# Kernel optimization log

Hardware: AMD Instinct MI355X
Metric: run time of the kernel (lower is better)

The kernel has to match this reference:

```python
import jax, jax.numpy as jnp
import numpy as np

B, S, H, HD = 2, 2048, 16, 128
HID = H * HD            # 2048
FF = 4 * HID            # 8192
ROT = int(HD * 0.25)    # 32 rotary dims (rotary_pct=0.25)
EPS = 1e-5
ROPE_BASE = 10000.0


def _layernorm(x, g, b):
    mu = jnp.mean(x, axis=-1, keepdims=True)
    var = jnp.mean(jnp.square(x - mu), axis=-1, keepdims=True)
    return (x - mu) * jax.lax.rsqrt(var + EPS) * g + b


def _rope_cos_sin(seq_len, dim, dtype):
    inv_freq = 1.0 / (ROPE_BASE ** (np.arange(0, dim, 2, dtype=np.float32) / dim))
    t = np.arange(seq_len, dtype=np.float32)
    freqs = np.outer(t, inv_freq)              # [S, dim/2]
    emb = np.concatenate([freqs, freqs], -1)   # [S, dim]
    return jnp.asarray(np.cos(emb), dtype), jnp.asarray(np.sin(emb), dtype)


def _apply_rope(x, cos, sin):
    # x: [B, H, S, ROT]; GPTNeoX rotate_half
    half = x.shape[-1] // 2
    x1, x2 = x[..., :half], x[..., half:]
    rot = jnp.concatenate([-x2, x1], axis=-1)
    return x * cos[None, None, :, :] + rot * sin[None, None, :, :]


def setup_inputs() -> dict:
    key = jax.random.key(0)
    ks = jax.random.split(key, 8)
    f = jnp.float32
    return {
        "hidden_states": jax.random.normal(ks[0], (B, S, HID), f),
        "ln1_g": jnp.ones((HID,), f), "ln1_b": jnp.zeros((HID,), f),
        "ln2_g": jnp.ones((HID,), f), "ln2_b": jnp.zeros((HID,), f),
        "W_qkv": jax.random.normal(ks[1], (HID, 3 * HID), f) * 0.02,
        "b_qkv": jnp.zeros((3 * HID,), f),
        "W_o": jax.random.normal(ks[2], (HID, HID), f) * 0.02,
        "b_o": jnp.zeros((HID,), f),
        "W_fc": jax.random.normal(ks[3], (HID, FF), f) * 0.02,
        "b_fc": jnp.zeros((FF,), f),
        "W_proj": jax.random.normal(ks[4], (FF, HID), f) * 0.02,
        "b_proj": jnp.zeros((HID,), f),
    }


def reference(hidden_states, ln1_g, ln1_b, ln2_g, ln2_b,
              W_qkv, b_qkv, W_o, b_o, W_fc, b_fc, W_proj, b_proj):
    dtype = hidden_states.dtype
    x = _layernorm(hidden_states, ln1_g, ln1_b)

    # fused QKV, GPTNeoX per-head interleaved layout [B,S,H,3*HD]
    qkv = (x @ W_qkv + b_qkv).reshape(B, S, H, 3 * HD)
    q = jnp.transpose(qkv[..., :HD], (0, 2, 1, 3))          # [B,H,S,HD]
    k = jnp.transpose(qkv[..., HD:2 * HD], (0, 2, 1, 3))
    v = jnp.transpose(qkv[..., 2 * HD:], (0, 2, 1, 3))

    cos, sin = _rope_cos_sin(S, ROT, dtype)
    q = jnp.concatenate([_apply_rope(q[..., :ROT], cos, sin), q[..., ROT:]], -1)
    k = jnp.concatenate([_apply_rope(k[..., :ROT], cos, sin), k[..., ROT:]], -1)

    # eager attention: scores / sqrt(hd), causal mask-fill, softmax, matmul
    scale = 1.0 / jnp.sqrt(jnp.asarray(HD, dtype))
    scores = jnp.einsum("bhqd,bhkd->bhqk", q, k) * scale
    causal = jnp.tril(jnp.ones((S, S), bool))
    scores = jnp.where(causal, scores, jnp.finfo(dtype).min)
    weights = jax.nn.softmax(scores, axis=-1)
    ctx = jnp.einsum("bhqk,bhkd->bhqd", weights, v)          # [B,H,S,HD]
    ctx = jnp.transpose(ctx, (0, 2, 1, 3)).reshape(B, S, HID)
    attn_out = ctx @ W_o + b_o

    # parallel residual: mlp(ln2(h)) + attn(ln1(h)) + h
    m = _layernorm(hidden_states, ln2_g, ln2_b)
    mlp_out = jax.nn.gelu(m @ W_fc + b_fc, approximate=False) @ W_proj + b_proj
    return mlp_out + attn_out + hidden_states
```

## Files before the change

### kernel.cpp

```cpp
#include <hip/hip_runtime.h>
#include <hip/hip_bf16.h>
#include <math.h>

#define BDIM 2
#define SDIM 2048
#define HDIM 16
#define HD 128
#define HID 2048
#define FFD 8192
#define NTOK (BDIM*SDIM)
#define QKVW (3*HID)

typedef __hip_bfloat16 bf16;
typedef __attribute__((ext_vector_type(8))) short short8;
typedef __attribute__((ext_vector_type(4))) short short4_;
typedef __attribute__((ext_vector_type(4))) float floatx4;

__device__ inline short bfbits(float f) {
  bf16 h = __float2bfloat16(f);
  short s;
  __builtin_memcpy(&s, &h, 2);
  return s;
}

__global__ __launch_bounds__(256) void transpose_cvt(
    const float* __restrict__ W, bf16* __restrict__ Wt, int K, int N)
{
  __shared__ float tile[32][33];
  int n0 = blockIdx.x * 32, k0 = blockIdx.y * 32;
  int tx = threadIdx.x, ty = threadIdx.y;
  #pragma unroll
  for (int r = ty; r < 32; r += 8)
    tile[r][tx] = W[(size_t)(k0 + r) * N + n0 + tx];
  __syncthreads();
  #pragma unroll
  for (int r = ty; r < 32; r += 8)
    Wt[(size_t)(n0 + r) * K + k0 + tx] = __float2bfloat16(tile[tx][r]);
}

__global__ __launch_bounds__(256) void ln_both(
    const float* __restrict__ x,
    const float* __restrict__ g1, const float* __restrict__ b1,
    const float* __restrict__ g2, const float* __restrict__ b2,
    bf16* __restrict__ o1, bf16* __restrict__ o2)
{
  int row = blockIdx.x;
  int tid = threadIdx.x;
  const float4* xr = (const float4*)(x + (size_t)row * HID);
  float4 va = xr[tid], vb = xr[tid + 256];
  float s = va.x + va.y + va.z + va.w + vb.x + vb.y + vb.z + vb.w;
  float q = va.x*va.x + va.y*va.y + va.z*va.z + va.w*va.w
          + vb.x*vb.x + vb.y*vb.y + vb.z*vb.z + vb.w*vb.w;
  #pragma unroll
  for (int off = 1; off < 64; off <<= 1) {
    s += __shfl_xor(s, off);
    q += __shfl_xor(q, off);
  }
  __shared__ float red[8];
  int wave = tid >> 6;
  if ((tid & 63) == 0) { red[wave] = s; red[4 + wave] = q; }
  __syncthreads();
  s = red[0] + red[1] + red[2] + red[3];
  q = red[4] + red[5] + red[6] + red[7];
  float mu = s * (1.0f / HID);
  float var = q * (1.0f / HID) - mu * mu;
  float rs = rsqrtf(var + 1e-5f);

  const float4* g1v = (const float4*)g1; const float4* b1v = (const float4*)b1;
  const float4* g2v = (const float4*)g2; const float4* b2v = (const float4*)b2;
  short4_* o1v = (short4_*)(o1 + (size_t)row * HID);
  short4_* o2v = (short4_*)(o2 + (size_t)row * HID);
  #pragma unroll
  for (int p = 0; p < 2; ++p) {
    int e = tid + p * 256;
    float4 xv = (p == 0) ? va : vb;
    float4 gv = g1v[e], bv = b1v[e];
    short4_ pk;
    pk[0] = bfbits((xv.x - mu) * rs * gv.x + bv.x);
    pk[1] = bfbits((xv.y - mu) * rs * gv.y + bv.y);
    pk[2] = bfbits((xv.z - mu) * rs * gv.z + bv.z);
    pk[3] = bfbits((xv.w - mu) * rs * gv.w + bv.w);
    o1v[e] = pk;
    gv = g2v[e]; bv = b2v[e];
    pk[0] = bfbits((xv.x - mu) * rs * gv.x + bv.x);
    pk[1] = bfbits((xv.y - mu) * rs * gv.y + bv.y);
    pk[2] = bfbits((xv.z - mu) * rs * gv.z + bv.z);
    pk[3] = bfbits((xv.w - mu) * rs * gv.w + bv.w);
    o2v[e] = pk;
  }
}

template<int EPI>
__global__ __launch_bounds__(512, 2) void gemm8(
    const bf16* __restrict__ A, const bf16* __restrict__ Bt,
    const float* __restrict__ bias,
    float* __restrict__ Cf, bf16* __restrict__ Cb,
    const bf16* __restrict__ r1b, const float* __restrict__ r2,
    int M, int N, int K)
{
  __shared__ bf16 SA[4][256 * 32];
  __shared__ bf16 SB[4][256 * 32];
  const int tid = threadIdx.x;
  const int wave = tid >> 6, lane = tid & 63;
  const int quad = lane >> 4, l16 = lane & 15;
  const int wr = wave >> 2, wc = wave & 3;

  const int nwg = gridDim.x * gridDim.y;
  const int flat = blockIdx.y * gridDim.x + blockIdx.x;
  const int swz = (flat & 7) * (nwg >> 3) + (flat >> 3);
  const int bx = swz % gridDim.x, by = swz / gridDim.x;
  const int n0 = bx * 256, m0 = by * 256;

  const int stg_r = wave * 16 + (lane >> 2);
  const int stg_c8 = (((lane & 3) ^ ((lane >> 3) & 3)) << 3);
  const bf16* stgA = A + (size_t)(m0 + stg_r) * K + stg_c8;
  const bf16* stgB = Bt + (size_t)(n0 + stg_r) * K + stg_c8;
  const int ldsOff = wave * 16 * 32;

  const int rd_sw = ((quad ^ ((l16 >> 1) & 3)) << 3);
  const int rdA = (wr * 128 + l16) * 32 + rd_sw;
  const int rdB = (wc * 64 + l16) * 32 + rd_sw;

  floatx4 acc[8][4];
  #pragma unroll
  for (int i = 0; i < 8; ++i)
    #pragma unroll
    for (int j = 0; j < 4; ++j) acc[i][j] = (floatx4)0.0f;

  const int KT = K >> 5;

#define STAGE_A8(KT3) { const int b_ = (KT3) & 3;                              \
  __builtin_amdgcn_global_load_lds(                                            \
      (const __attribute__((address_space(1))) void*)(stgA + (size_t)(KT3)*32),\
      (__attribute__((address_space(3))) void*)&SA[b_][ldsOff], 16, 0, 0);     \
  __builtin_amdgcn_global_load_lds(                                            \
      (const __attribute__((address_space(1))) void*)(stgA + (size_t)128*K + (size_t)(KT3)*32), \
      (__attribute__((address_space(3))) void*)&SA[b_][128*32 + ldsOff], 16, 0, 0); }
#define STAGE_B8(KT3) { const int b_ = (KT3) & 3;                              \
  __builtin_amdgcn_global_load_lds(                                            \
      (const __attribute__((address_space(1))) void*)(stgB + (size_t)(KT3)*32),\
      (__attribute__((address_space(3))) void*)&SB[b_][ldsOff], 16, 0, 0);     \
  __builtin_amdgcn_global_load_lds(                                            \
      (const __attribute__((address_space(1))) void*)(stgB + (size_t)128*K + (size_t)(KT3)*32), \
      (__attribute__((address_space(3))) void*)&SB[b_][128*32 + ldsOff], 16, 0, 0); }

  STAGE_A8(0); STAGE_B8(0);
  STAGE_A8(1); STAGE_B8(1);
  STAGE_A8(2); STAGE_B8(2);
  asm volatile("s_waitcnt vmcnt(8)" ::: "memory");
  __builtin_amdgcn_s_barrier();

  short8 av[4], bv[4];
  for (int kt = 0; kt < KT; ++kt) {
    const bf16* as_ = &SA[kt & 3][0];
    const bf16* bs_ = &SB[kt & 3][0];
    const bool st = (kt + 3) < KT;

    #pragma unroll
    for (int i = 0; i < 4; ++i) av[i] = *(const short8*)&as_[rdA + i * 512];
    #pragma unroll
    for (int j = 0; j < 4; ++j) bv[j] = *(const short8*)&bs_[rdB + j * 512];
    if (st) STAGE_A8(kt + 3);
    __builtin_amdgcn_s_barrier();
    asm volatile("s_waitcnt lgkmcnt(0)" ::: "memory");
    __builtin_amdgcn_sched_barrier(0);
    __builtin_amdgcn_s_setprio(1);
    #pragma unroll
    for (int i = 0; i < 4; ++i)
      #pragma unroll
      for (int j = 0; j < 4; ++j)
        acc[i][j] = __builtin_amdgcn_mfma_f32_16x16x32_bf16(av[i], bv[j], acc[i][j], 0, 0, 0);
    __builtin_amdgcn_s_setprio(0);
    __builtin_amdgcn_s_barrier();

    #pragma unroll
    for (int i = 0; i < 4; ++i) av[i] = *(const short8*)&as_[rdA + 2048 + i * 512];
    if (st) STAGE_B8(kt + 3);
    __builtin_amdgcn_s_barrier();
    asm volatile("s_waitcnt lgkmcnt(0)" ::: "memory");
    __builtin_amdgcn_sched_barrier(0);
    __builtin_amdgcn_s_setprio(1);
    #pragma unroll
    for (int i = 0; i < 4; ++i)
      #pragma unroll
      for (int j = 0; j < 4; ++j)
        acc[4 + i][j] = __builtin_amdgcn_mfma_f32_16x16x32_bf16(av[i], bv[j], acc[4 + i][j], 0, 0, 0);
    __builtin_amdgcn_s_setprio(0);

    if (st) {
      asm volatile("s_waitcnt vmcnt(8)" ::: "memory");
    } else if (kt + 3 == KT) {
      asm volatile("s_waitcnt vmcnt(4)" ::: "memory");
    } else if (kt + 2 == KT) {
      asm volatile("s_waitcnt vmcnt(0)" ::: "memory");
    }
    if (kt + 1 < KT) __builtin_amdgcn_s_barrier();
  }
#undef STAGE_A8
#undef STAGE_B8

  #pragma unroll
  for (int i = 0; i < 8; ++i) {
    #pragma unroll
    for (int j = 0; j < 4; ++j) {
      int col = n0 + wc * 64 + j * 16 + l16;
      float bsv = bias[col];
      #pragma unroll
      for (int r = 0; r < 4; ++r) {
        int row = m0 + wr * 128 + i * 16 + quad * 4 + r;
        size_t idx = (size_t)row * N + col;
        float v = acc[i][j][r] + bsv;
        if (EPI == 1) {
          v = 0.5f * v * (1.0f + erff(v * 0.70710678118654752f));
          Cb[idx] = __float2bfloat16(v);
        } else if (EPI == 2) {
          Cf[idx] = v + __bfloat162float(r1b[idx]) + r2[idx];
        } else {
          Cb[idx] = __float2bfloat16(v);
        }
      }
    }
  }
}

__global__ __launch_bounds__(256) void rope_vt(
    bf16* __restrict__ qkv, bf16* __restrict__ vT)
{
  int bh = blockIdx.x, s0 = blockIdx.y * 32;
  int b = bh >> 4, h = bh & 15;
  int tid = threadIdx.x;
  __shared__ bf16 vs[32][136];
  const float qsc = 0.12751740f;

  for (int idx = tid; idx < 512; idx += 256) {
    int sl = idx >> 4, d = idx & 15;
    int s = s0 + sl;
    bf16* base = qkv + (size_t)(b * SDIM + s) * QKVW + h * 384;
    float fr = (float)s * expf(-(float)d * 0.5756462732485114f);
    float c = cosf(fr), sn = sinf(fr);
    float q1 = __bfloat162float(base[d]);
    float q2 = __bfloat162float(base[d + 16]);
    float k1 = __bfloat162float(base[128 + d]);
    float k2 = __bfloat162float(base[128 + d + 16]);
    base[d]        = __float2bfloat16(qsc * (q1 * c - q2 * sn));
    base[d + 16]   = __float2bfloat16(qsc * (q2 * c + q1 * sn));
    base[128 + d]      = __float2bfloat16(k1 * c - k2 * sn);
    base[128 + d + 16] = __float2bfloat16(k2 * c + k1 * sn);
  }
  for (int idx = tid; idx < 32 * 96; idx += 256) {
    int sl = idx / 96, d = 32 + idx % 96;
    bf16* base = qkv + (size_t)(b * SDIM + s0 + sl) * QKVW + h * 384;
    base[d] = __float2bfloat16(qsc * __bfloat162float(base[d]));
  }

  for (int idx = tid; idx < 32 * 128; idx += 256) {
    int sl = idx >> 7, d = idx & 127;
    vs[sl][d] = qkv[(size_t)(b * SDIM + s0 + sl) * QKVW + h * 384 + 256 + d];
  }
  __syncthreads();
  for (int idx = tid; idx < 32 * 128; idx += 256) {
    int d = idx >> 5, sl = idx & 31;
    vT[((size_t)bh * HD + d) * SDIM + s0 + sl] = vs[sl][d];
  }
}

#define LOAD_K(KB, K0) { \
  int krow_ = (K0); \
  _Pragma("unroll") for (int nh_ = 0; nh_ < 2; ++nh_) \
    _Pragma("unroll") for (int c_ = 0; c_ < 4; ++c_) \
      KB[nh_*4+c_] = *(const short8*)&Kb[(size_t)(krow_ + nh_*16 + l16) * QKVW + c_*32 + quad*8]; }

#define SOFTMAX(S0, S1, MR, LR, OO, ROWQ, DOMASK, K0, SLOT) { \
  if (DOMASK) { \
    _Pragma("unroll") for (int r_ = 0; r_ < 4; ++r_) { \
      int row_ = (ROWQ) + quad*4 + r_; \
      S0[r_] = ((K0) + l16 <= row_) ? S0[r_] : -1e30f; \
      S1[r_] = ((K0) + 16 + l16 <= row_) ? S1[r_] : -1e30f; } } \
  _Pragma("unroll") for (int r_ = 0; r_ < 4; ++r_) { \
    float mx_ = fmaxf(S0[r_], S1[r_]); \
    mx_ = fmaxf(mx_, __shfl_xor(mx_, 1)); \
    mx_ = fmaxf(mx_, __shfl_xor(mx_, 2)); \
    mx_ = fmaxf(mx_, __shfl_xor(mx_, 4)); \
    mx_ = fmaxf(mx_, __shfl_xor(mx_, 8)); \
    float mnew_ = fmaxf(MR[r_], mx_); \
    float alpha_ = __builtin_amdgcn_exp2f(MR[r_] - mnew_); \
    MR[r_] = mnew_; \
    S0[r_] = __builtin_amdgcn_exp2f(S0[r_] - mnew_); \
    S1[r_] = __builtin_amdgcn_exp2f(S1[r_] - mnew_); \
    float sm_ = S0[r_] + S1[r_]; \
    sm_ += __shfl_xor(sm_, 1); sm_ += __shfl_xor(sm_, 2); \
    sm_ += __shfl_xor(sm_, 4); sm_ += __shfl_xor(sm_, 8); \
    LR[r_] = LR[r_] * alpha_ + sm_; \
    _Pragma("unroll") for (int d_ = 0; d_ < 8; ++d_) OO[d_][r_] *= alpha_; \
    Ps[wave][SLOT][quad*4 + r_][l16]      = __float2bfloat16(S0[r_]); \
    Ps[wave][SLOT][quad*4 + r_][16 + l16] = __float2bfloat16(S1[r_]); } }

#define FLASH_ITER(IT, KC, KN) { \
  const int k0_ = (IT) * 32; \
  const int k0n_ = ((IT) + 1 < nk) ? k0_ + 32 : 0; \
  LOAD_K(KN, k0n_); \
  short8 vbuf_[8]; \
  _Pragma("unroll") for (int d_ = 0; d_ < 8; ++d_) \
    vbuf_[d_] = *(const short8*)&Vb[(size_t)(d_*16 + l16) * SDIM + k0_ + quad*8]; \
  floatx4 scB_[2]; scB_[0] = (floatx4)0.0f; scB_[1] = (floatx4)0.0f; \
  _Pragma("unroll") for (int c_ = 0; c_ < 4; ++c_) { \
    scB_[0] = __builtin_amdgcn_mfma_f32_16x16x32_bf16(aqB[c_], KC[c_],   scB_[0], 0,0,0); \
    scB_[1] = __builtin_amdgcn_mfma_f32_16x16x32_bf16(aqB[c_], KC[4+c_], scB_[1], 0,0,0); } \
  const bool actA_ = (k0_ <= qa + 15); \
  floatx4 scA_[2]; scA_[0] = (floatx4)0.0f; scA_[1] = (floatx4)0.0f; \
  if (actA_) { \
    _Pragma("unroll") for (int c_ = 0; c_ < 4; ++c_) { \
      scA_[0] = __builtin_amdgcn_mfma_f32_16x16x32_bf16(aqA[c_], KC[c_],   scA_[0], 0,0,0); \
      scA_[1] = __builtin_amdgcn_mfma_f32_16x16x32_bf16(aqA[c_], KC[4+c_], scA_[1], 0,0,0); } } \
  SOFTMAX(scB_[0], scB_[1], mB, lB, oB, qb, (k0_ + 32 >= kmax), k0_, 0); \
  if (actA_) { \
    SOFTMAX(scA_[0], scA_[1], mA, lA, oA, qa, (k0_ + 32 > qa + 15), k0_, 1); \
    short8 pfB_ = *(const short8*)&Ps[wave][0][l16][quad*8]; \
    short8 pfA_ = *(const short8*)&Ps[wave][1][l16][quad*8]; \
    _Pragma("unroll") for (int d_ = 0; d_ < 8; ++d_) { \
      oB[d_] = __builtin_amdgcn_mfma_f32_16x16x32_bf16(pfB_, vbuf_[d_], oB[d_], 0,0,0); \
      oA[d_] = __builtin_amdgcn_mfma_f32_16x16x32_bf16(pfA_, vbuf_[d_], oA[d_], 0,0,0); } \
  } else { \
    short8 pfB_ = *(const short8*)&Ps[wave][0][l16][quad*8]; \
    _Pragma("unroll") for (int d_ = 0; d_ < 8; ++d_) \
      oB[d_] = __builtin_amdgcn_mfma_f32_16x16x32_bf16(pfB_, vbuf_[d_], oB[d_], 0,0,0); } }

__global__ __launch_bounds__(256) void flash_attn(
    const bf16* __restrict__ qkv, const bf16* __restrict__ vT,
    bf16* __restrict__ ctx)
{
  int bh = blockIdx.x;
  int b = bh >> 4, h = bh & 15;
  int tid = threadIdx.x;
  int wave = tid >> 6, lane = tid & 63;
  int quad = lane >> 4, l16 = lane & 15;
  int p = blockIdx.y * 4 + wave;
  int qa = 16 * p;
  int qb = SDIM - 16 * (p + 1);
  int kmax = qb + 16;
  int nk = (kmax + 31) >> 5;
  const bf16* Qb = qkv + (size_t)b * SDIM * QKVW + h * 384;
  const bf16* Kb = Qb + 128;
  const bf16* Vb = vT + (size_t)bh * HD * SDIM;
  __shared__ bf16 Ps[4][2][16][32];

  short8 aqA[4], aqB[4];
  #pragma unroll
  for (int c = 0; c < 4; ++c) {
    aqA[c] = *(const short8*)&Qb[(size_t)(qa + l16) * QKVW + c * 32 + quad * 8];
    aqB[c] = *(const short8*)&Qb[(size_t)(qb + l16) * QKVW + c * 32 + quad * 8];
  }

  floatx4 oA[8], oB[8];
  #pragma unroll
  for (int d = 0; d < 8; ++d) { oA[d] = (floatx4)0.0f; oB[d] = (floatx4)0.0f; }
  float mA[4] = {-INFINITY, -INFINITY, -INFINITY, -INFINITY};
  float mB[4] = {-INFINITY, -INFINITY, -INFINITY, -INFINITY};
  float lA[4] = {0.0f, 0.0f, 0.0f, 0.0f};
  float lB[4] = {0.0f, 0.0f, 0.0f, 0.0f};

  short8 kb0[8], kb1[8];
  LOAD_K(kb0, 0);
  for (int it = 0; it < nk; it += 2) {
    FLASH_ITER(it, kb0, kb1);
    if (it + 1 < nk) { FLASH_ITER(it + 1, kb1, kb0); }
  }

  float rlA[4], rlB[4];
  #pragma unroll
  for (int r = 0; r < 4; ++r) { rlA[r] = 1.0f / lA[r]; rlB[r] = 1.0f / lB[r]; }
  #pragma unroll
  for (int d = 0; d < 8; ++d) {
    #pragma unroll
    for (int r = 0; r < 4; ++r) {
      int rowA = qa + quad * 4 + r;
      int rowB = qb + quad * 4 + r;
      ctx[((size_t)b * SDIM + rowA) * HID + h * HD + d * 16 + l16] =
          __float2bfloat16(oA[d][r] * rlA[r]);
      ctx[((size_t)b * SDIM + rowB) * HID + h * HD + d * 16 + l16] =
          __float2bfloat16(oB[d][r] * rlB[r]);
    }
  }
}

extern "C" void kernel_launch(void* const* d_in, const int* in_sizes, int n_in,
                              void* d_out, int out_size, void* d_ws, size_t ws_size,
                              hipStream_t stream) {
  const float* hidden = (const float*)d_in[0];
  const float* ln1g = (const float*)d_in[1];
  const float* ln1b = (const float*)d_in[2];
  const float* ln2g = (const float*)d_in[3];
  const float* ln2b = (const float*)d_in[4];
  const float* Wqkv = (const float*)d_in[5];
  const float* bqkv = (const float*)d_in[6];
  const float* Wo   = (const float*)d_in[7];
  const float* bo   = (const float*)d_in[8];
  const float* Wfc  = (const float*)d_in[9];
  const float* bfc  = (const float*)d_in[10];
  const float* Wproj= (const float*)d_in[11];
  const float* bproj= (const float*)d_in[12];

  char* ws = (char*)d_ws;
  const size_t SZ_WQKV = (size_t)QKVW * HID * 2;
  const size_t SZ_WO   = (size_t)HID * HID * 2;
  const size_t SZ_WFC  = (size_t)FFD * HID * 2;
  const size_t SZ_WPROJ= (size_t)HID * FFD * 2;
  const size_t SZ_ACT  = (size_t)NTOK * HID * 2;
  const size_t SZ_QKV  = (size_t)NTOK * QKVW * 2;

  bf16* wqkvT = (bf16*)(ws + 0);
  bf16* woT   = (bf16*)(ws + SZ_WQKV);
  bf16* wfcT  = (bf16*)(ws + SZ_WQKV + SZ_WO);
  bf16* wprojT= (bf16*)(ws + SZ_WQKV + SZ_WO + SZ_WFC);
  char* actbase = ws + SZ_WQKV + SZ_WO + SZ_WFC + SZ_WPROJ;
  bf16* xln   = (bf16*)(actbase);
  bf16* mln   = (bf16*)(actbase + SZ_ACT);
  bf16* qkvb  = (bf16*)(actbase + 2 * SZ_ACT);
  bf16* vT    = (bf16*)(actbase + 2 * SZ_ACT + SZ_QKV);
  bf16* ctx   = xln;
  bf16* attnb = wqkvT;
  bf16* hfc   = qkvb;

  dim3 tblk(32, 8);
  transpose_cvt<<<dim3(QKVW / 32, HID / 32), tblk, 0, stream>>>(Wqkv, wqkvT, HID, QKVW);
  transpose_cvt<<<dim3(HID / 32, HID / 32), tblk, 0, stream>>>(Wo, woT, HID, HID);
  transpose_cvt<<<dim3(FFD / 32, HID / 32), tblk, 0, stream>>>(Wfc, wfcT, HID, FFD);
  transpose_cvt<<<dim3(HID / 32, FFD / 32), tblk, 0, stream>>>(Wproj, wprojT, FFD, HID);

  ln_both<<<NTOK, 256, 0, stream>>>(hidden, ln1g, ln1b, ln2g, ln2b, xln, mln);

  gemm8<3><<<dim3(QKVW / 256, NTOK / 256), 512, 0, stream>>>(
      xln, wqkvT, bqkv, nullptr, qkvb, nullptr, nullptr, NTOK, QKVW, HID);

  rope_vt<<<dim3(32, SDIM / 32), 256, 0, stream>>>(qkvb, vT);

  flash_attn<<<dim3(32, SDIM / 128), 256, 0, stream>>>(qkvb, vT, ctx);

  gemm8<3><<<dim3(HID / 256, NTOK / 256), 512, 0, stream>>>(
      ctx, woT, bo, nullptr, attnb, nullptr, nullptr, NTOK, HID, HID);

  gemm8<1><<<dim3(FFD / 256, NTOK / 256), 512, 0, stream>>>(
      mln, wfcT, bfc, nullptr, hfc, nullptr, nullptr, NTOK, FFD, HID);

  gemm8<2><<<dim3(HID / 256, NTOK / 256), 512, 0, stream>>>(
      hfc, wprojT, bproj, (float*)d_out, nullptr, attnb, hidden, NTOK, HID, FFD);
}
```

Before: 1.120 ms.

## Template GEMM on M-tile height and use 128-row tiles for smaller GEMMs

Adds a BM template parameter to the bf16 GEMM so the M tile can be 128 rows instead of 256. The QKV, output-projection and down-projection GEMMs switch to 128-row tiles, which doubles their workgroup count so the grid fills more of the GPU's compute units. The main loop is also reorganised: A and B stages are issued together, and the barriers between the two MFMA halves are removed. Trade-off: less reuse of B per tile and more total global traffic, and fewer barriers could risk LDS races if the 4-stage buffering margin does not cover them.

```diff
diff --git a/kernel.cpp b/kernel.cpp
--- a/kernel.cpp
+++ b/kernel.cpp
@@ -90,7 +90,7 @@
   }
 }
 
-template<int EPI>
+template<int EPI, int BM>
 __global__ __launch_bounds__(512, 2) void gemm8(
     const bf16* __restrict__ A, const bf16* __restrict__ Bt,
     const float* __restrict__ bias,
@@ -98,7 +98,8 @@
     const bf16* __restrict__ r1b, const float* __restrict__ r2,
     int M, int N, int K)
 {
-  __shared__ bf16 SA[4][256 * 32];
+  constexpr int NI = BM / 32;
+  __shared__ bf16 SA[4][BM * 32];
   __shared__ bf16 SB[4][256 * 32];
   const int tid = threadIdx.x;
   const int wave = tid >> 6, lane = tid & 63;
@@ -109,7 +110,7 @@
   const int flat = blockIdx.y * gridDim.x + blockIdx.x;
   const int swz = (flat & 7) * (nwg >> 3) + (flat >> 3);
   const int bx = swz % gridDim.x, by = swz / gridDim.x;
-  const int n0 = bx * 256, m0 = by * 256;
+  const int n0 = bx * 256, m0 = by * BM;
 
   const int stg_r = wave * 16 + (lane >> 2);
   const int stg_c8 = (((lane & 3) ^ ((lane >> 3) & 3)) << 3);
@@ -118,12 +119,12 @@
   const int ldsOff = wave * 16 * 32;
 
   const int rd_sw = ((quad ^ ((l16 >> 1) & 3)) << 3);
-  const int rdA = (wr * 128 + l16) * 32 + rd_sw;
+  const int rdA = (wr * (BM / 2) + l16) * 32 + rd_sw;
   const int rdB = (wc * 64 + l16) * 32 + rd_sw;
 
-  floatx4 acc[8][4];
-  #pragma unroll
-  for (int i = 0; i < 8; ++i)
+  floatx4 acc[NI][4];
+  #pragma unroll
+  for (int i = 0; i < NI; ++i)
     #pragma unroll
     for (int j = 0; j < 4; ++j) acc[i][j] = (floatx4)0.0f;
 
@@ -133,9 +134,10 @@
   __builtin_amdgcn_global_load_lds(                                            \
       (const __attribute__((address_space(1))) void*)(stgA + (size_t)(KT3)*32),\
       (__attribute__((address_space(3))) void*)&SA[b_][ldsOff], 16, 0, 0);     \
-  __builtin_amdgcn_global_load_lds(                                            \
-      (const __attribute__((address_space(1))) void*)(stgA + (size_t)128*K + (size_t)(KT3)*32), \
-      (__attribute__((address_space(3))) void*)&SA[b_][128*32 + ldsOff], 16, 0, 0); }
+  if constexpr (BM == 256) {                                                   \
+    __builtin_amdgcn_global_load_lds(                                          \
+        (const __attribute__((address_space(1))) void*)(stgA + (size_t)128*K + (size_t)(KT3)*32), \
+        (__attribute__((address_space(3))) void*)&SA[b_][128*32 + ldsOff], 16, 0, 0); } }
 #define STAGE_B8(KT3) { const int b_ = (KT3) & 3;                              \
   __builtin_amdgcn_global_load_lds(                                            \
       (const __attribute__((address_space(1))) void*)(stgB + (size_t)(KT3)*32),\
@@ -147,21 +149,21 @@
   STAGE_A8(0); STAGE_B8(0);
   STAGE_A8(1); STAGE_B8(1);
   STAGE_A8(2); STAGE_B8(2);
-  asm volatile("s_waitcnt vmcnt(8)" ::: "memory");
+  if constexpr (BM == 256) asm volatile("s_waitcnt vmcnt(8)" ::: "memory");
+  else                     asm volatile("s_waitcnt vmcnt(6)" ::: "memory");
   __builtin_amdgcn_s_barrier();
 
-  short8 av[4], bv[4];
   for (int kt = 0; kt < KT; ++kt) {
     const bf16* as_ = &SA[kt & 3][0];
     const bf16* bs_ = &SB[kt & 3][0];
     const bool st = (kt + 3) < KT;
 
+    short8 av[4], bv[4];
     #pragma unroll
     for (int i = 0; i < 4; ++i) av[i] = *(const short8*)&as_[rdA + i * 512];
     #pragma unroll
     for (int j = 0; j < 4; ++j) bv[j] = *(const short8*)&bs_[rdB + j * 512];
-    if (st) STAGE_A8(kt + 3);
-    __builtin_amdgcn_s_barrier();
+    if (st) { STAGE_A8(kt + 3); STAGE_B8(kt + 3); }
     asm volatile("s_waitcnt lgkmcnt(0)" ::: "memory");
     __builtin_amdgcn_sched_barrier(0);
     __builtin_amdgcn_s_setprio(1);
@@ -171,26 +173,27 @@
       for (int j = 0; j < 4; ++j)
         acc[i][j] = __builtin_amdgcn_mfma_f32_16x16x32_bf16(av[i], bv[j], acc[i][j], 0, 0, 0);
     __builtin_amdgcn_s_setprio(0);
-    __builtin_amdgcn_s_barrier();
-
-    #pragma unroll
-    for (int i = 0; i < 4; ++i) av[i] = *(const short8*)&as_[rdA + 2048 + i * 512];
-    if (st) STAGE_B8(kt + 3);
-    __builtin_amdgcn_s_barrier();
-    asm volatile("s_waitcnt lgkmcnt(0)" ::: "memory");
-    __builtin_amdgcn_sched_barrier(0);
-    __builtin_amdgcn_s_setprio(1);
-    #pragma unroll
-    for (int i = 0; i < 4; ++i)
+
+    if constexpr (BM == 256) {
       #pragma unroll
-      for (int j = 0; j < 4; ++j)
-        acc[4 + i][j] = __builtin_amdgcn_mfma_f32_16x16x32_bf16(av[i], bv[j], acc[4 + i][j], 0, 0, 0);
-    __builtin_amdgcn_s_setprio(0);
+      for (int i = 0; i < 4; ++i) av[i] = *(const short8*)&as_[rdA + 2048 + i * 512];
+      asm volatile("s_waitcnt lgkmcnt(0)" ::: "memory");
+      __builtin_amdgcn_sched_barrier(0);
+      __builtin_amdgcn_s_setprio(1);
+      #pragma unroll
+      for (int i = 0; i < 4; ++i)
+        #pragma unroll
+        for (int j = 0; j < 4; ++j)
+          acc[4 + i][j] = __builtin_amdgcn_mfma_f32_16x16x32_bf16(av[i], bv[j], acc[4 + i][j], 0, 0, 0);
+      __builtin_amdgcn_s_setprio(0);
+    }
 
     if (st) {
-      asm volatile("s_waitcnt vmcnt(8)" ::: "memory");
+      if constexpr (BM == 256) asm volatile("s_waitcnt vmcnt(8)" ::: "memory");
+      else                     asm volatile("s_waitcnt vmcnt(6)" ::: "memory");
     } else if (kt + 3 == KT) {
-      asm volatile("s_waitcnt vmcnt(4)" ::: "memory");
+      if constexpr (BM == 256) asm volatile("s_waitcnt vmcnt(4)" ::: "memory");
+      else                     asm volatile("s_waitcnt vmcnt(3)" ::: "memory");
     } else if (kt + 2 == KT) {
       asm volatile("s_waitcnt vmcnt(0)" ::: "memory");
     }
@@ -200,14 +203,14 @@
 #undef STAGE_B8
 
   #pragma unroll
-  for (int i = 0; i < 8; ++i) {
+  for (int i = 0; i < NI; ++i) {
     #pragma unroll
     for (int j = 0; j < 4; ++j) {
       int col = n0 + wc * 64 + j * 16 + l16;
       float bsv = bias[col];
       #pragma unroll
       for (int r = 0; r < 4; ++r) {
-        int row = m0 + wr * 128 + i * 16 + quad * 4 + r;
+        int row = m0 + wr * (BM / 2) + i * 16 + quad * 4 + r;
         size_t idx = (size_t)row * N + col;
         float v = acc[i][j][r] + bsv;
         if (EPI == 1) {
@@ -429,19 +432,19 @@
 
   ln_both<<<NTOK, 256, 0, stream>>>(hidden, ln1g, ln1b, ln2g, ln2b, xln, mln);
 
-  gemm8<3><<<dim3(QKVW / 256, NTOK / 256), 512, 0, stream>>>(
+  gemm8<3, 128><<<dim3(QKVW / 256, NTOK / 128), 512, 0, stream>>>(
       xln, wqkvT, bqkv, nullptr, qkvb, nullptr, nullptr, NTOK, QKVW, HID);
 
   rope_vt<<<dim3(32, SDIM / 32), 256, 0, stream>>>(qkvb, vT);
 
   flash_attn<<<dim3(32, SDIM / 128), 256, 0, stream>>>(qkvb, vT, ctx);
 
-  gemm8<3><<<dim3(HID / 256, NTOK / 256), 512, 0, stream>>>(
+  gemm8<3, 128><<<dim3(HID / 256, NTOK / 128), 512, 0, stream>>>(
       ctx, woT, bo, nullptr, attnb, nullptr, nullptr, NTOK, HID, HID);
 
-  gemm8<1><<<dim3(FFD / 256, NTOK / 256), 512, 0, stream>>>(
+  gemm8<1, 256><<<dim3(FFD / 256, NTOK / 256), 512, 0, stream>>>(
       mln, wfcT, bfc, nullptr, hfc, nullptr, nullptr, NTOK, FFD, HID);
 
-  gemm8<2><<<dim3(HID / 256, NTOK / 256), 512, 0, stream>>>(
+  gemm8<2, 128><<<dim3(HID / 256, NTOK / 128), 512, 0, stream>>>(
       hfc, wprojT, bproj, (float*)d_out, nullptr, attnb, hidden, NTOK, HID, FFD);
 }
```

After: 1.116 ms. Within noise of the previous version (-0.3%).
